# Kernel tuning notes

Hardware: AMD Instinct MI355X
Metric: run time of the kernel (lower is better)

The kernel has to match this reference:

```python
import jax, jax.numpy as jnp
import numpy as np

N_NODES = 100000
N_EDGES = 1600000
IN_SIZE, HID_SIZE, OUT_SIZE = 128, 64, 64


def _glorot(key, shape):
    lim = float(np.sqrt(6.0 / (shape[0] + shape[1])))
    return jax.random.uniform(key, shape, jnp.float32, -lim, lim)


def setup_inputs() -> dict:
    key = jax.random.key(0)
    ks = jax.random.split(key, 6)
    features = jax.random.normal(ks[0], (N_NODES, IN_SIZE), jnp.float32)
    src = jax.random.randint(ks[1], (N_EDGES,), 0, N_NODES)
    dst = jax.random.randint(ks[2], (N_EDGES,), 0, N_NODES)
    return {
        "features": features,
        "W0": _glorot(ks[3], (IN_SIZE, HID_SIZE)),
        "b0": jnp.zeros((HID_SIZE,), jnp.float32),
        "W1": _glorot(ks[4], (HID_SIZE, HID_SIZE)),
        "b1": jnp.zeros((HID_SIZE,), jnp.float32),
        "W2": _glorot(ks[5], (HID_SIZE, OUT_SIZE)),
        "b2": jnp.zeros((OUT_SIZE,), jnp.float32),
        "src": src,
        "dst": dst,
    }


def reference(features, W0, b0, W1, b1, W2, b2, src, dst):
    # DGL GraphConv with norm='both': h' = relu(D_in^{-1/2} A D_out^{-1/2} h W + b)
    # Dropout layers are identity in eval mode (deterministic baseline).
    N = features.shape[0]
    ones = jnp.ones(src.shape, features.dtype)
    deg_out = jax.ops.segment_sum(ones, src, num_segments=N)
    deg_in = jax.ops.segment_sum(ones, dst, num_segments=N)
    norm_src = jnp.where(deg_out > 0, deg_out, 1.0) ** -0.5  # [N]
    norm_dst = jnp.where(deg_in > 0, deg_in, 1.0) ** -0.5    # [N]

    def layer(h, W, b):
        h = h * norm_src[:, None]          # source-side degree norm
        m = (h @ W)[src]                   # project first (in >= out), then gather [E, d_out]
        agg = jax.ops.segment_sum(m, dst, num_segments=N)  # scatter-add to destinations
        return jax.nn.relu(agg * norm_dst[:, None] + b)

    h = layer(features, W0, b0)
    h = layer(h, W1, b1)
    return layer(h, W2, b2)
```

## Files before the change

kernel.cpp:

```cpp
#include <hip/hip_runtime.h>
#include <hip/hip_bf16.h>

typedef __hip_bfloat16 bf16;
typedef __attribute__((ext_vector_type(8))) short bf16x8;
typedef __attribute__((ext_vector_type(8))) unsigned short u16x8;
typedef __attribute__((ext_vector_type(4))) float f32x4;
typedef __attribute__((ext_vector_type(4))) int i32x4;
typedef __attribute__((ext_vector_type(4))) short s16x4;

__device__ __forceinline__ float b2f(unsigned short u) {
  return __uint_as_float(((unsigned)u) << 16);
}
__device__ __forceinline__ unsigned short f2b(float x) {
  bf16 h = __float2bfloat16(x);
  return *reinterpret_cast<unsigned short*>(&h);
}

__global__ void __launch_bounds__(1024) k_passA(
    const int* __restrict__ src, const int* __restrict__ dst, int E,
    int nbuck, int M, int* __restrict__ counts,
    const unsigned short* __restrict__ raw, int* __restrict__ flag) {
  const int t = threadIdx.x;
  if (blockIdx.x == 256) {
    __shared__ int sbad, snz;
    if (t == 0) { sbad = 0; snz = 0; }
    __syncthreads();
    if (t < 256) {
      const unsigned short u = raw[t];
      const float a = fabsf(b2f(u));
      if (!(a < 100.f)) atomicAdd(&sbad, 1);
      if (((t & 1) == 0) && u != 0) atomicAdd(&snz, 1);
    }
    __syncthreads();
    if (t == 0) flag[0] = (sbad == 0 && snz > 0) ? 1 : 0;
    return;
  }
  extern __shared__ int lh[];
  int* lh1 = lh;
  int* lh2 = lh + nbuck;
  for (int k = t; k < 2 * nbuck; k += 1024) lh[k] = 0;
  __syncthreads();
  const int chunk = (E + 255) / 256;
  const int s = blockIdx.x * chunk;
  const int e = min(E, s + chunk);
  for (int i = s + t; i < e; i += 1024) {
    atomicAdd(&lh1[dst[i] >> 8], 1);
    atomicAdd(&lh2[src[i] >> 8], 1);
  }
  __syncthreads();
  for (int k = t; k < nbuck; k += 1024) {
    counts[k * 256 + blockIdx.x] = lh1[k];
    counts[M + k * 256 + blockIdx.x] = lh2[k];
  }
}

__global__ void k_scan1(const int* __restrict__ a, int M2, int* __restrict__ bsums) {
  __shared__ int sdata[256];
  int i = blockIdx.x * 256 + threadIdx.x;
  int v = (i < M2) ? a[i] : 0;
  sdata[threadIdx.x] = v;
  __syncthreads();
  for (int s = 128; s > 0; s >>= 1) {
    if (threadIdx.x < s) sdata[threadIdx.x] += sdata[threadIdx.x + s];
    __syncthreads();
  }
  if (threadIdx.x == 0) bsums[blockIdx.x] = sdata[0];
}

__global__ void __launch_bounds__(1024) k_scan2(
    int* __restrict__ bsums, int nb, int* __restrict__ rowStart, int N, int E,
    const void* __restrict__ W1, const void* __restrict__ W2,
    const int* __restrict__ flag,
    unsigned short* __restrict__ WT1, unsigned short* __restrict__ WT2) {
  const int t = threadIdx.x;
  if (blockIdx.x > 0) {
    const int i = (blockIdx.x - 1) * 1024 + t;
    if (i < 8192) {
      const bool isb = (*flag != 0);
      const int j = i & 4095;
      const int n = j >> 6, k = j & 63;
      const void* W = (i < 4096) ? W1 : W2;
      unsigned short* WT = (i < 4096) ? WT1 : WT2;
      const float v = isb ? b2f(((const unsigned short*)W)[k * 64 + n])
                          : ((const float*)W)[k * 64 + n];
      WT[j] = f2b(v);
    }
    return;
  }
  __shared__ int s[1024];
  const int v = (t < nb) ? bsums[t] : 0;
  s[t] = v;
  __syncthreads();
  for (int off = 1; off < 1024; off <<= 1) {
    int u = (t >= off) ? s[t - off] : 0;
    __syncthreads();
    s[t] += u;
    __syncthreads();
  }
  if (t < nb) bsums[t] = s[t] - v;
  if (t == 0) rowStart[N] = E;
}

__global__ void k_scan3(int* __restrict__ a, int M2, const int* __restrict__ bsums) {
  __shared__ int sdata[256];
  int i = blockIdx.x * 256 + threadIdx.x;
  int v = (i < M2) ? a[i] : 0;
  sdata[threadIdx.x] = v;
  __syncthreads();
  for (int off = 1; off < 256; off <<= 1) {
    int t = (threadIdx.x >= off) ? sdata[threadIdx.x - off] : 0;
    __syncthreads();
    sdata[threadIdx.x] += t;
    __syncthreads();
  }
  if (i < M2) a[i] = bsums[blockIdx.x] + sdata[threadIdx.x] - v;
}

__global__ void __launch_bounds__(1024) k_passC(
    const int* __restrict__ src, const int* __restrict__ dst, int E,
    int nbuck, int M, const int* __restrict__ S,
    int* __restrict__ tmp, unsigned char* __restrict__ tmp2) {
  extern __shared__ int cur[];
  int* cur1 = cur;
  int* cur2 = cur + nbuck;
  const int t = threadIdx.x;
  for (int k = t; k < nbuck; k += 1024) {
    cur1[k] = S[k * 256 + blockIdx.x];
    cur2[k] = S[M + k * 256 + blockIdx.x];
  }
  __syncthreads();
  const int chunk = (E + 255) / 256;
  const int s = blockIdx.x * chunk;
  const int e = min(E, s + chunk);
  for (int i = s + t; i < e; i += 1024) {
    const int sv = src[i];
    const int d = dst[i];
    const int pos1 = atomicAdd(&cur1[d >> 8], 1);
    tmp[pos1] = sv | ((d & 255) << 20);
    const int pos2 = atomicAdd(&cur2[sv >> 8], 1);
    tmp2[pos2 - E] = (unsigned char)(sv & 255);
  }
}

__global__ void __launch_bounds__(1024) k_passD(
    const int* __restrict__ tmp, const unsigned char* __restrict__ tmp2,
    const int* __restrict__ S, int nbuck, int M, int N, int E,
    int* __restrict__ rowStart, int* __restrict__ edgeSrc,
    float* __restrict__ ns, float* __restrict__ nd) {
  __shared__ int h[256];
  __shared__ int ex[256];
  __shared__ int c[256];
  const int t = threadIdx.x;
  const int k = blockIdx.x;
  const int node = k * 256 + t;
  const int bs2 = S[M + k * 256] - E;
  const int be2 = (k + 1 < nbuck) ? (S[M + (k + 1) * 256] - E) : E;
  if (t < 256) h[t] = 0;
  __syncthreads();
  for (int i = bs2 + t; i < be2; i += 1024) atomicAdd(&h[tmp2[i]], 1);
  __syncthreads();
  if (t < 256 && node < N) {
    int dov = h[t];
    if (dov <= 0) dov = 1;
    ns[node] = rsqrtf((float)dov);
  }
  __syncthreads();
  const int bs = S[k * 256];
  const int be = (k + 1 < nbuck) ? S[(k + 1) * 256] : E;
  if (t < 256) h[t] = 0;
  __syncthreads();
  for (int i = bs + t; i < be; i += 1024) atomicAdd(&h[tmp[i] >> 20], 1);
  __syncthreads();
  int cnt = 0;
  if (t < 256) {
    cnt = h[t];
    ex[t] = cnt;
  }
  __syncthreads();
  for (int off = 1; off < 256; off <<= 1) {
    int u = (t < 256 && t >= off) ? ex[t - off] : 0;
    __syncthreads();
    if (t < 256) ex[t] += u;
    __syncthreads();
  }
  if (t < 256) {
    const int excl = ex[t] - cnt;
    if (node < N) {
      rowStart[node] = bs + excl;
      nd[node] = rsqrtf((float)(cnt > 0 ? cnt : 1));
    }
    c[t] = bs + excl;
  }
  __syncthreads();
  for (int i = bs + t; i < be; i += 1024) {
    const int v = tmp[i];
    const int pos = atomicAdd(&c[v >> 20], 1);
    edgeSrc[pos] = v & 0xFFFFF;
  }
}

template <int K, bool FIRST, bool SCALE>
__device__ __forceinline__ void gemm_loadA(const void* hin, bool isb, int rowA,
                                           int quad, bf16x8* A) {
  constexpr int KT = K / 32;
  if (FIRST && !isb) {
    const float* hp = (const float*)hin + (size_t)rowA * K;
#pragma unroll
    for (int kt = 0; kt < KT; ++kt) {
      const float4 u0 = *(const float4*)(hp + kt * 32 + quad * 8);
      const float4 u1 = *(const float4*)(hp + kt * 32 + quad * 8 + 4);
      A[kt][0] = (short)f2b(u0.x); A[kt][1] = (short)f2b(u0.y);
      A[kt][2] = (short)f2b(u0.z); A[kt][3] = (short)f2b(u0.w);
      A[kt][4] = (short)f2b(u1.x); A[kt][5] = (short)f2b(u1.y);
      A[kt][6] = (short)f2b(u1.z); A[kt][7] = (short)f2b(u1.w);
    }
  } else {
    const unsigned short* hp = (const unsigned short*)hin + (size_t)rowA * K;
#pragma unroll
    for (int kt = 0; kt < KT; ++kt)
      A[kt] = *(const bf16x8*)(hp + kt * 32 + quad * 8);
  }
}

template <int K, bool FIRST, bool SCALE>
__global__ void __launch_bounds__(256) k_gemm(
    const void* __restrict__ hin, const void* __restrict__ Wv,
    const int* __restrict__ flag, const float* __restrict__ norm_src,
    int N, unsigned short* __restrict__ out) {
  constexpr int KT = K / 32;
  constexpr int ST = K + 8;
  constexpr int CST = 72;
  __shared__ unsigned short Wl[64 * ST];
  __shared__ unsigned short Cl[4][16 * CST];
  const bool isb = (*flag != 0);
  const int tid = threadIdx.x;
  const int lane = tid & 63;
  const int quad = lane >> 4;
  const int l16 = lane & 15;
  const int w = tid >> 6;

  const int wid = blockIdx.x * 4 + w;
  const int nw = gridDim.x * 4;
  const int G = (N + 15) >> 4;
  const int g1 = wid + nw;

  bf16x8 A[2][KT];
  {
    const int r0 = min((wid << 4) + l16, N - 1);
    const int r1 = min((g1 << 4) + l16, N - 1);
    gemm_loadA<K, FIRST, SCALE>(hin, isb, r0, quad, A[0]);
    gemm_loadA<K, FIRST, SCALE>(hin, isb, r1, quad, A[1]);
  }

  {
    const unsigned short* Wus = (const unsigned short*)Wv;
    const float* Wf = (const float*)Wv;
    for (int i0 = tid * 8; i0 < K * 64; i0 += 2048) {
      const int k = i0 >> 6;
      const int n0 = i0 & 63;
      unsigned short v[8];
      if (isb) {
        const u16x8 u = *(const u16x8*)(Wus + i0);
#pragma unroll
        for (int j = 0; j < 8; ++j) v[j] = u[j];
      } else {
        const float4 f0 = *(const float4*)(Wf + i0);
        const float4 f1 = *(const float4*)(Wf + i0 + 4);
        v[0] = f2b(f0.x); v[1] = f2b(f0.y); v[2] = f2b(f0.z); v[3] = f2b(f0.w);
        v[4] = f2b(f1.x); v[5] = f2b(f1.y); v[6] = f2b(f1.z); v[7] = f2b(f1.w);
      }
#pragma unroll
      for (int j = 0; j < 8; ++j) Wl[(n0 + j) * ST + k] = v[j];
    }
  }
  __syncthreads();

  unsigned short* myC = &Cl[w][0];
#pragma unroll
  for (int gi = 0; gi < 2; ++gi) {
    const int g = (gi == 0) ? wid : g1;
    f32x4 acc[4] = {{0.f, 0.f, 0.f, 0.f}, {0.f, 0.f, 0.f, 0.f},
                    {0.f, 0.f, 0.f, 0.f}, {0.f, 0.f, 0.f, 0.f}};
#pragma unroll
    for (int kt = 0; kt < KT; ++kt) {
      const int koff = kt * 32 + quad * 8;
#pragma unroll
      for (int nt = 0; nt < 4; ++nt) {
        const bf16x8 Bf = *(const bf16x8*)&Wl[(nt * 16 + l16) * ST + koff];
        acc[nt] = __builtin_amdgcn_mfma_f32_16x16x32_bf16(A[gi][kt], Bf, acc[nt], 0, 0, 0);
      }
    }
    const int rowD = quad * 4;
#pragma unroll
    for (int r = 0; r < 4; ++r) {
      const int nodeW = min((g << 4) + rowD + r, N - 1);
      const float f = SCALE ? norm_src[nodeW] : 1.0f;
#pragma unroll
      for (int nt = 0; nt < 4; ++nt)
        myC[(rowD + r) * CST + nt * 16 + l16] = f2b(SCALE ? acc[nt][r] * f : acc[nt][r]);
    }
    __builtin_amdgcn_sched_barrier(0);
    const int row2 = lane >> 2;
    const int c0 = (lane & 3) * 16;
    const int node = (g << 4) + row2;
    if (node < N) {
      const u16x8 v0 = *(const u16x8*)&myC[row2 * CST + c0];
      const u16x8 v1 = *(const u16x8*)&myC[row2 * CST + c0 + 8];
      *(u16x8*)(out + (size_t)node * 64 + c0) = v0;
      *(u16x8*)(out + (size_t)node * 64 + c0 + 8) = v1;
    }
  }
}

__device__ __forceinline__ void agg_chunk_compute(unsigned trbase, int cb32, int lo,
                                                  unsigned span, int quad, f32x4* acc) {
  const int posbase = cb32 + (quad << 2);
  const unsigned u0 = (unsigned)(posbase - lo);
  bf16x8 Af;
#pragma unroll
  for (int j = 0; j < 8; ++j) {
    const unsigned off = (j < 4) ? (unsigned)j : (unsigned)(12 + j);
    Af[j] = ((u0 + off) < span) ? (short)0x3F80 : (short)0;
  }
  s16x4 t0[4], t1[4];
#pragma unroll
  for (int nt = 0; nt < 4; ++nt) {
    const unsigned a = trbase + (unsigned)(nt * 1024);
    asm volatile("ds_read_b64_tr_b16 %0, %1" : "=v"(t0[nt]) : "v"(a) : "memory");
    asm volatile("ds_read_b64_tr_b16 %0, %1 offset:512" : "=v"(t1[nt]) : "v"(a) : "memory");
  }
  asm volatile("s_waitcnt lgkmcnt(0)" ::: "memory");
  __builtin_amdgcn_sched_barrier(0);
#pragma unroll
  for (int nt = 0; nt < 4; ++nt) {
    bf16x8 Bf;
    Bf[0] = t0[nt][0]; Bf[1] = t0[nt][1]; Bf[2] = t0[nt][2]; Bf[3] = t0[nt][3];
    Bf[4] = t1[nt][0]; Bf[5] = t1[nt][1]; Bf[6] = t1[nt][2]; Bf[7] = t1[nt][3];
    acc[nt] = __builtin_amdgcn_mfma_f32_16x16x32_bf16(Af, Bf, acc[nt], 0, 0, 0);
  }
}

template <bool LAST, bool FUSE>
__global__ void __launch_bounds__(256) k_aggregate(
    const unsigned short* __restrict__ proj,
    const int* __restrict__ edgeSrc, const int* __restrict__ rowStart,
    const float* __restrict__ norm_dst, const float* __restrict__ norm_src,
    const void* __restrict__ bias, const int* __restrict__ flag,
    const unsigned short* __restrict__ WT, int N, int E, void* __restrict__ outp) {
  __shared__ unsigned short lds[4][2048];
  const bool isb = (*flag != 0);
  const int tid = threadIdx.x;
  const int w = tid >> 6;
  const int lane = tid & 63;
  const int l16 = lane & 15;
  const int quad = lane >> 4;
  const int e32 = lane & 31;
  const int p = lane >> 5;

  const int wid = blockIdx.x * 4 + w;
  const int g0 = wid * 8;

  float bcol[4];
#pragma unroll
  for (int nt = 0; nt < 4; ++nt) {
    const int col = nt * 16 + l16;
    bcol[nt] = isb ? b2f(((const unsigned short*)bias)[col]) : ((const float*)bias)[col];
  }

  const int cb = rowStart[min(g0, N)];
  const int ce = rowStart[min(g0 + 8, N)];
  const int L = ce - cb;
  const int nch = (L + 31) >> 5;

  const int rsi = min(g0 + min(l16, 8), N);
  const int rsj = min(g0 + min(l16 + 1, 8), N);
  const int lo = rowStart[rsi];
  const unsigned span = (unsigned)(rowStart[rsj] - lo);

  int idxc[6];
#pragma unroll
  for (int t = 0; t < 6; ++t) {
    const int pos = min(cb + t * 32 + e32, E - 1);
    idxc[t] = edgeSrc[pos];
  }

  unsigned short* myl = &lds[w][0];
  unsigned wofs[4];
#pragma unroll
  for (int q = 0; q < 4; ++q) {
    const int n0 = p * 32 + q * 8;
    wofs[q] = (unsigned)((n0 >> 4) * 512 + e32 * 16 + (n0 & 15));
  }
  const unsigned trbase = (unsigned)(uintptr_t)myl + (unsigned)lane * 8u;

  f32x4 acc[4] = {{0.f, 0.f, 0.f, 0.f}, {0.f, 0.f, 0.f, 0.f},
                  {0.f, 0.f, 0.f, 0.f}, {0.f, 0.f, 0.f, 0.f}};

  i32x4 gb[2][4];
#define AGG_ISSUE(t, b)                                                         \
  {                                                                             \
    const unsigned short* rp = proj + (size_t)idxc[t] * 64 + p * 32;            \
    gb[b][0] = *(const i32x4*)(rp);                                             \
    gb[b][1] = *(const i32x4*)(rp + 8);                                         \
    gb[b][2] = *(const i32x4*)(rp + 16);                                        \
    gb[b][3] = *(const i32x4*)(rp + 24);                                        \
  }
  if (0 < nch) AGG_ISSUE(0, 0);
  if (1 < nch) AGG_ISSUE(1, 1);

#pragma unroll
  for (int tt = 0; tt < 6; ++tt) {
    if (tt < nch) {
#pragma unroll
      for (int q = 0; q < 4; ++q) *(i32x4*)(myl + wofs[q]) = gb[tt & 1][q];
      if (tt + 2 < 6 && tt + 2 < nch) AGG_ISSUE(tt + 2, tt & 1);
      asm volatile("s_waitcnt lgkmcnt(0)" ::: "memory");
      agg_chunk_compute(trbase, cb + tt * 32, lo, span, quad, acc);
    }
  }
  for (int t = 6; t < nch; ++t) {
    const int pos = min(cb + t * 32 + e32, E - 1);
    const int idx = edgeSrc[pos];
    const unsigned short* rp = proj + (size_t)idx * 64 + p * 32;
    i32x4 g4[4];
    g4[0] = *(const i32x4*)(rp);
    g4[1] = *(const i32x4*)(rp + 8);
    g4[2] = *(const i32x4*)(rp + 16);
    g4[3] = *(const i32x4*)(rp + 24);
#pragma unroll
    for (int q = 0; q < 4; ++q) *(i32x4*)(myl + wofs[q]) = g4[q];
    asm volatile("s_waitcnt lgkmcnt(0)" ::: "memory");
    agg_chunk_compute(trbase, cb + t * 32, lo, span, quad, acc);
  }
#undef AGG_ISSUE

  if constexpr (FUSE) {
    __syncthreads();
    unsigned short* hT = &lds[0][0];
    const int r0 = (w & 1) * 16;
    const int cb2 = (w >> 1) * 32;
    bf16x8 Bfr[2][2];
#pragma unroll
    for (int kt = 0; kt < 2; ++kt) {
      const int koff = kt * 32 + quad * 8;
#pragma unroll
      for (int nt = 0; nt < 2; ++nt)
        Bfr[kt][nt] = *(const bf16x8*)(WT + (size_t)(cb2 + nt * 16 + l16) * 64 + koff);
    }
#pragma unroll
    for (int reg = 0; reg < 4; ++reg) {
      const int row = quad * 4 + reg;
      if (row < 8) {
        const int node = min(g0 + row, N - 1);
        const float nd = norm_dst[node];
        const float esc = norm_src[node];
#pragma unroll
        for (int nt = 0; nt < 4; ++nt) {
          const float x = fmaxf(fmaf(acc[nt][reg], nd, bcol[nt]), 0.f) * esc;
          hT[(w * 8 + row) * 72 + nt * 16 + l16] = f2b(x);
        }
      }
    }
    __syncthreads();
    bf16x8 Afr[2];
#pragma unroll
    for (int kt = 0; kt < 2; ++kt)
      Afr[kt] = *(const bf16x8*)&hT[(r0 + l16) * 72 + kt * 32 + quad * 8];
    f32x4 acc2[2] = {{0.f, 0.f, 0.f, 0.f}, {0.f, 0.f, 0.f, 0.f}};
#pragma unroll
    for (int kt = 0; kt < 2; ++kt)
#pragma unroll
      for (int nt = 0; nt < 2; ++nt)
        acc2[nt] = __builtin_amdgcn_mfma_f32_16x16x32_bf16(Afr[kt], Bfr[kt][nt], acc2[nt], 0, 0, 0);
    __syncthreads();
#pragma unroll
    for (int nt = 0; nt < 2; ++nt)
#pragma unroll
      for (int reg = 0; reg < 4; ++reg) {
        const int row = r0 + quad * 4 + reg;
        hT[row * 72 + cb2 + nt * 16 + l16] = f2b(acc2[nt][reg]);
      }
    __syncthreads();
    const int row = tid >> 3;
    const int c0 = (tid & 7) * 8;
    const int node = blockIdx.x * 32 + row;
    if (node < N) {
      *(u16x8*)((unsigned short*)outp + (size_t)node * 64 + c0) =
          *(const u16x8*)&hT[row * 72 + c0];
    }
  } else {
    if (!isb) {
      float* fs = (float*)myl;
#pragma unroll
      for (int reg = 0; reg < 4; ++reg) {
        const int row = quad * 4 + reg;
        if (row < 8) {
          const int node = min(g0 + row, N - 1);
          const float nd = norm_dst[node];
#pragma unroll
          for (int nt = 0; nt < 4; ++nt)
            fs[row * 64 + nt * 16 + l16] = fmaxf(fmaf(acc[nt][reg], nd, bcol[nt]), 0.f);
        }
      }
      asm volatile("s_waitcnt lgkmcnt(0)" ::: "memory");
      __builtin_amdgcn_sched_barrier(0);
      const int r = lane >> 3;
      const int c0 = (lane & 7) * 8;
      const int node = g0 + r;
      if (node < N) {
        const float4 v0 = *(const float4*)&fs[r * 64 + c0];
        const float4 v1 = *(const float4*)&fs[r * 64 + c0 + 4];
        float* of = (float*)outp + (size_t)node * 64 + c0;
        *(float4*)of = v0;
        *(float4*)(of + 4) = v1;
      }
    } else {
#pragma unroll
      for (int reg = 0; reg < 4; ++reg) {
        const int row = quad * 4 + reg;
        if (row < 8) {
          const int node = min(g0 + row, N - 1);
          const float nd = norm_dst[node];
#pragma unroll
          for (int nt = 0; nt < 4; ++nt) {
            const float x = fmaxf(fmaf(acc[nt][reg], nd, bcol[nt]), 0.f);
            myl[row * 64 + nt * 16 + l16] = f2b(x);
          }
        }
      }
      asm volatile("s_waitcnt lgkmcnt(0)" ::: "memory");
      __builtin_amdgcn_sched_barrier(0);
      if (lane < 32) {
        const int r = lane >> 2;
        const int c0 = (lane & 3) * 16;
        const int node = g0 + r;
        if (node < N) {
          const u16x8 v0 = *(const u16x8*)&myl[r * 64 + c0];
          const u16x8 v1 = *(const u16x8*)&myl[r * 64 + c0 + 8];
          *(u16x8*)((unsigned short*)outp + (size_t)node * 64 + c0) = v0;
          *(u16x8*)((unsigned short*)outp + (size_t)node * 64 + c0 + 8) = v1;
        }
      }
    }
  }
}

extern "C" void kernel_launch(void* const* d_in, const int* in_sizes, int n_in,
                              void* d_out, int out_size, void* d_ws, size_t ws_size,
                              hipStream_t stream) {
  const void* features = d_in[0];
  const void* W0 = d_in[1];
  const void* b0 = d_in[2];
  const void* W1 = d_in[3];
  const void* b1 = d_in[4];
  const void* W2 = d_in[5];
  const void* b2 = d_in[6];
  const int* src = (const int*)d_in[7];
  const int* dst = (const int*)d_in[8];
  const int N = in_sizes[0] / 128;
  const int E = in_sizes[7];
  const int NBUCK = (N + 255) >> 8;
  const int M = NBUCK * 256;
  const int M2 = 2 * M;

  char* w = (char*)d_ws;
  size_t off = 0;
  auto alloc = [&](size_t bytes) {
    void* p = w + off;
    off = (off + bytes + 255) & ~(size_t)255;
    return p;
  };
  int* flag = (int*)alloc(4);
  int* rowStart = (int*)alloc((size_t)(N + 1) * 4);
  int* counts = (int*)alloc((size_t)M2 * 4);
  int* bsums = (int*)alloc(1024 * 4);
  float* norm_src = (float*)alloc((size_t)N * 4);
  float* norm_dst = (float*)alloc((size_t)N * 4);
  int* tmp = (int*)alloc((size_t)E * 4);
  unsigned char* tmp2 = (unsigned char*)alloc((size_t)E);
  int* edgeSrc = (int*)alloc((size_t)E * 4);
  unsigned short* projA = (unsigned short*)alloc((size_t)N * 64 * 2);
  unsigned short* projB = (unsigned short*)alloc((size_t)N * 64 * 2);
  unsigned short* WT1 = (unsigned short*)alloc(64 * 64 * 2);
  unsigned short* WT2 = (unsigned short*)alloc(64 * 64 * 2);

  const size_t lds_nb = (size_t)NBUCK * 2 * 4;
  const int G16 = (N + 15) / 16;
  const int GB = (G16 + 7) / 8;

  k_passA<<<257, 1024, lds_nb, stream>>>(src, dst, E, NBUCK, M, counts,
                                         (const unsigned short*)features, flag);
  const int NB2 = (M2 + 255) / 256;
  k_scan1<<<NB2, 256, 0, stream>>>(counts, M2, bsums);
  k_scan2<<<9, 1024, 0, stream>>>(bsums, NB2, rowStart, N, E, W1, W2, flag, WT1, WT2);
  k_scan3<<<NB2, 256, 0, stream>>>(counts, M2, bsums);
  k_passC<<<256, 1024, lds_nb, stream>>>(src, dst, E, NBUCK, M, counts, tmp, tmp2);
  k_passD<<<NBUCK, 1024, 0, stream>>>(tmp, tmp2, counts, NBUCK, M, N, E,
                                      rowStart, edgeSrc, norm_src, norm_dst);

  const int AB = (((N + 7) / 8) + 3) / 4;
  k_gemm<128, true, true><<<GB, 256, 0, stream>>>(features, W0, flag, norm_src, N, projA);
  k_aggregate<false, true><<<AB, 256, 0, stream>>>(projA, edgeSrc, rowStart, norm_dst,
                                                   norm_src, b0, flag, WT1, N, E, projB);
  k_aggregate<false, true><<<AB, 256, 0, stream>>>(projB, edgeSrc, rowStart, norm_dst,
                                                   norm_src, b1, flag, WT2, N, E, projA);
  k_aggregate<true, false><<<AB, 256, 0, stream>>>(projA, edgeSrc, rowStart, norm_dst,
                                                   norm_src, b2, flag, nullptr, N, E, d_out);
}
```

Baseline: 289.3 us.

## Replicate LDS histograms per thread group and give each GEMM wave one tile

The bucket histograms in passA and the per-node degree histograms in passD are split into four replicas, one per group of 256 threads, and summed at the end. This is meant to reduce contention on LDS atomics. The first-layer GEMM now gives each wave a single 16-row tile instead of two, doubling the grid so more waves run in parallel. The cost is more LDS per block in passA, which may lower occupancy, plus redundant weight staging across the extra blocks.

```diff
diff --git a/kernel.cpp b/kernel.cpp
--- a/kernel.cpp
+++ b/kernel.cpp
@@ -36,21 +36,24 @@
     return;
   }
   extern __shared__ int lh[];
-  int* lh1 = lh;
-  int* lh2 = lh + nbuck;
-  for (int k = t; k < 2 * nbuck; k += 1024) lh[k] = 0;
+  const int rep = t >> 8;
+  int* l1 = lh + rep * 2 * nbuck;
+  int* l2 = l1 + nbuck;
+  for (int k = t; k < 8 * nbuck; k += 1024) lh[k] = 0;
   __syncthreads();
   const int chunk = (E + 255) / 256;
   const int s = blockIdx.x * chunk;
   const int e = min(E, s + chunk);
   for (int i = s + t; i < e; i += 1024) {
-    atomicAdd(&lh1[dst[i] >> 8], 1);
-    atomicAdd(&lh2[src[i] >> 8], 1);
+    atomicAdd(&l1[dst[i] >> 8], 1);
+    atomicAdd(&l2[src[i] >> 8], 1);
   }
   __syncthreads();
   for (int k = t; k < nbuck; k += 1024) {
-    counts[k * 256 + blockIdx.x] = lh1[k];
-    counts[M + k * 256 + blockIdx.x] = lh2[k];
+    counts[k * 256 + blockIdx.x] =
+        lh[k] + lh[2 * nbuck + k] + lh[4 * nbuck + k] + lh[6 * nbuck + k];
+    counts[M + k * 256 + blockIdx.x] =
+        lh[nbuck + k] + lh[3 * nbuck + k] + lh[5 * nbuck + k] + lh[7 * nbuck + k];
   }
 }
 
@@ -147,33 +150,34 @@
     const int* __restrict__ S, int nbuck, int M, int N, int E,
     int* __restrict__ rowStart, int* __restrict__ edgeSrc,
     float* __restrict__ ns, float* __restrict__ nd) {
-  __shared__ int h[256];
+  __shared__ int h[4][256];
   __shared__ int ex[256];
   __shared__ int c[256];
   const int t = threadIdx.x;
   const int k = blockIdx.x;
   const int node = k * 256 + t;
+  const int rep = t >> 8;
   const int bs2 = S[M + k * 256] - E;
   const int be2 = (k + 1 < nbuck) ? (S[M + (k + 1) * 256] - E) : E;
-  if (t < 256) h[t] = 0;
-  __syncthreads();
-  for (int i = bs2 + t; i < be2; i += 1024) atomicAdd(&h[tmp2[i]], 1);
+  if (t < 256) { h[0][t] = 0; h[1][t] = 0; h[2][t] = 0; h[3][t] = 0; }
+  __syncthreads();
+  for (int i = bs2 + t; i < be2; i += 1024) atomicAdd(&h[rep][tmp2[i]], 1);
   __syncthreads();
   if (t < 256 && node < N) {
-    int dov = h[t];
+    int dov = h[0][t] + h[1][t] + h[2][t] + h[3][t];
     if (dov <= 0) dov = 1;
     ns[node] = rsqrtf((float)dov);
   }
   __syncthreads();
   const int bs = S[k * 256];
   const int be = (k + 1 < nbuck) ? S[(k + 1) * 256] : E;
-  if (t < 256) h[t] = 0;
-  __syncthreads();
-  for (int i = bs + t; i < be; i += 1024) atomicAdd(&h[tmp[i] >> 20], 1);
+  if (t < 256) { h[0][t] = 0; h[1][t] = 0; h[2][t] = 0; h[3][t] = 0; }
+  __syncthreads();
+  for (int i = bs + t; i < be; i += 1024) atomicAdd(&h[rep][tmp[i] >> 20], 1);
   __syncthreads();
   int cnt = 0;
   if (t < 256) {
-    cnt = h[t];
+    cnt = h[0][t] + h[1][t] + h[2][t] + h[3][t];
     ex[t] = cnt;
   }
   __syncthreads();
@@ -239,17 +243,13 @@
   const int l16 = lane & 15;
   const int w = tid >> 6;
 
-  const int wid = blockIdx.x * 4 + w;
-  const int nw = gridDim.x * 4;
+  const int g = blockIdx.x * 4 + w;
   const int G = (N + 15) >> 4;
-  const int g1 = wid + nw;
-
-  bf16x8 A[2][KT];
+
+  bf16x8 A[KT];
   {
-    const int r0 = min((wid << 4) + l16, N - 1);
-    const int r1 = min((g1 << 4) + l16, N - 1);
-    gemm_loadA<K, FIRST, SCALE>(hin, isb, r0, quad, A[0]);
-    gemm_loadA<K, FIRST, SCALE>(hin, isb, r1, quad, A[1]);
+    const int r0 = min((g << 4) + l16, N - 1);
+    gemm_loadA<K, FIRST, SCALE>(hin, isb, r0, quad, A);
   }
 
   {
@@ -274,41 +274,38 @@
     }
   }
   __syncthreads();
+  if (g >= G) return;
 
   unsigned short* myC = &Cl[w][0];
-#pragma unroll
-  for (int gi = 0; gi < 2; ++gi) {
-    const int g = (gi == 0) ? wid : g1;
-    f32x4 acc[4] = {{0.f, 0.f, 0.f, 0.f}, {0.f, 0.f, 0.f, 0.f},
-                    {0.f, 0.f, 0.f, 0.f}, {0.f, 0.f, 0.f, 0.f}};
-#pragma unroll
-    for (int kt = 0; kt < KT; ++kt) {
-      const int koff = kt * 32 + quad * 8;
-#pragma unroll
-      for (int nt = 0; nt < 4; ++nt) {
-        const bf16x8 Bf = *(const bf16x8*)&Wl[(nt * 16 + l16) * ST + koff];
-        acc[nt] = __builtin_amdgcn_mfma_f32_16x16x32_bf16(A[gi][kt], Bf, acc[nt], 0, 0, 0);
-      }
-    }
-    const int rowD = quad * 4;
-#pragma unroll
-    for (int r = 0; r < 4; ++r) {
-      const int nodeW = min((g << 4) + rowD + r, N - 1);
-      const float f = SCALE ? norm_src[nodeW] : 1.0f;
-#pragma unroll
-      for (int nt = 0; nt < 4; ++nt)
-        myC[(rowD + r) * CST + nt * 16 + l16] = f2b(SCALE ? acc[nt][r] * f : acc[nt][r]);
-    }
-    __builtin_amdgcn_sched_barrier(0);
-    const int row2 = lane >> 2;
-    const int c0 = (lane & 3) * 16;
-    const int node = (g << 4) + row2;
-    if (node < N) {
-      const u16x8 v0 = *(const u16x8*)&myC[row2 * CST + c0];
-      const u16x8 v1 = *(const u16x8*)&myC[row2 * CST + c0 + 8];
-      *(u16x8*)(out + (size_t)node * 64 + c0) = v0;
-      *(u16x8*)(out + (size_t)node * 64 + c0 + 8) = v1;
-    }
+  f32x4 acc[4] = {{0.f, 0.f, 0.f, 0.f}, {0.f, 0.f, 0.f, 0.f},
+                  {0.f, 0.f, 0.f, 0.f}, {0.f, 0.f, 0.f, 0.f}};
+#pragma unroll
+  for (int kt = 0; kt < KT; ++kt) {
+    const int koff = kt * 32 + quad * 8;
+#pragma unroll
+    for (int nt = 0; nt < 4; ++nt) {
+      const bf16x8 Bf = *(const bf16x8*)&Wl[(nt * 16 + l16) * ST + koff];
+      acc[nt] = __builtin_amdgcn_mfma_f32_16x16x32_bf16(A[kt], Bf, acc[nt], 0, 0, 0);
+    }
+  }
+  const int rowD = quad * 4;
+#pragma unroll
+  for (int r = 0; r < 4; ++r) {
+    const int nodeW = min((g << 4) + rowD + r, N - 1);
+    const float f = SCALE ? norm_src[nodeW] : 1.0f;
+#pragma unroll
+    for (int nt = 0; nt < 4; ++nt)
+      myC[(rowD + r) * CST + nt * 16 + l16] = f2b(SCALE ? acc[nt][r] * f : acc[nt][r]);
+  }
+  __builtin_amdgcn_sched_barrier(0);
+  const int row2 = lane >> 2;
+  const int c0 = (lane & 3) * 16;
+  const int node = (g << 4) + row2;
+  if (node < N) {
+    const u16x8 v0 = *(const u16x8*)&myC[row2 * CST + c0];
+    const u16x8 v1 = *(const u16x8*)&myC[row2 * CST + c0 + 8];
+    *(u16x8*)(out + (size_t)node * 64 + c0) = v0;
+    *(u16x8*)(out + (size_t)node * 64 + c0 + 8) = v1;
   }
 }
 
@@ -584,17 +581,18 @@
   unsigned short* WT1 = (unsigned short*)alloc(64 * 64 * 2);
   unsigned short* WT2 = (unsigned short*)alloc(64 * 64 * 2);
 
-  const size_t lds_nb = (size_t)NBUCK * 2 * 4;
+  const size_t lds_nbA = (size_t)NBUCK * 2 * 4 * 4;
+  const size_t lds_nbC = (size_t)NBUCK * 2 * 4;
   const int G16 = (N + 15) / 16;
-  const int GB = (G16 + 7) / 8;
-
-  k_passA<<<257, 1024, lds_nb, stream>>>(src, dst, E, NBUCK, M, counts,
-                                         (const unsigned short*)features, flag);
+  const int GB = (G16 + 3) / 4;
+
+  k_passA<<<257, 1024, lds_nbA, stream>>>(src, dst, E, NBUCK, M, counts,
+                                          (const unsigned short*)features, flag);
   const int NB2 = (M2 + 255) / 256;
   k_scan1<<<NB2, 256, 0, stream>>>(counts, M2, bsums);
   k_scan2<<<9, 1024, 0, stream>>>(bsums, NB2, rowStart, N, E, W1, W2, flag, WT1, WT2);
   k_scan3<<<NB2, 256, 0, stream>>>(counts, M2, bsums);
-  k_passC<<<256, 1024, lds_nb, stream>>>(src, dst, E, NBUCK, M, counts, tmp, tmp2);
+  k_passC<<<256, 1024, lds_nbC, stream>>>(src, dst, E, NBUCK, M, counts, tmp, tmp2);
   k_passD<<<NBUCK, 1024, 0, stream>>>(tmp, tmp2, counts, NBUCK, M, N, E,
                                       rowStart, edgeSrc, norm_src, norm_dst);
 
```

New measurement: 289.7 us. No clear change (+0.1%).
